# Optimization experiments

Hardware: AMD Instinct MI355X
Metric: run time of the kernel (lower is better)

## Reference

```python
import jax, jax.numpy as jnp
import numpy as np

B, T, S, F, D, M = 8, 8192, 8192, 64, 64, 128
EPS = 1e-9


def _draw_omega(n_omega, d_feature, rng):
    # Stacked orthogonal blocks scaled by sqrt(d_feature), as in the TF module.
    n_blocks = (n_omega + d_feature - 1) // d_feature + 1
    blocks = []
    for _ in range(n_blocks):
        g = rng.standard_normal((d_feature, d_feature)).astype(np.float32)
        q, _ = np.linalg.qr(g)
        blocks.append(q * np.sqrt(float(d_feature)))
    return jnp.asarray(np.concatenate(blocks, axis=0)[:n_omega])


def setup_inputs() -> dict:
    k0 = jax.random.key(0)
    kq, kv, kk = jax.random.split(k0, 3)
    query = jax.random.normal(kq, (B, T, F), dtype=jnp.float32)
    value = jax.random.normal(kv, (B, S, D), dtype=jnp.float32)
    key = jax.random.normal(kk, (B, S, F), dtype=jnp.float32)
    omega = _draw_omega(M, F, np.random.default_rng(0))  # (M, F)
    return {"query": query, "value": value, "key": key, "omega": omega}


def _phi(x, omega):
    # x: (B, L, F) -> (B, L, 2M) positive random features
    m = omega.shape[0]
    square_sum = jnp.sum(x * x, axis=-1, keepdims=True) / 2.0  # (B, L, 1)
    xw = jnp.einsum('blf,mf->blm', x, omega)                   # (B, L, M)
    unnorm = jnp.exp(jnp.concatenate([xw, -xw], axis=-1) - square_sum) + EPS
    return unnorm / jnp.sqrt(2.0 * m)


def reference(query, value, key, omega):
    q = _phi(query, omega)  # (B, T, 2M)
    k = _phi(key, omega)    # (B, S, 2M)
    ones = jnp.ones(value.shape[:-1] + (1,), dtype=value.dtype)
    v1 = jnp.concatenate([value, ones], axis=-1)               # (B, S, D+1)
    kv = jnp.einsum('bsm,bsd->bmd', k, v1)                     # (B, 2M, D+1)
    qkv = jnp.einsum('btm,bmd->btd', q, kv)                    # (B, T, D+1)
    normalizer = qkv[:, :, -1:]
    return qkv[:, :, :-1] / normalizer
```

## Files before the change

kernel.cpp:

```cpp
#include <hip/hip_runtime.h>


constexpr int NB = 8;
constexpr int NT = 8192;
constexpr float EPSF = 1e-9f;
constexpr float SCALE = 0.0625f;

typedef short s8v __attribute__((ext_vector_type(8)));
typedef short s4v __attribute__((ext_vector_type(4)));
typedef float f4v __attribute__((ext_vector_type(4)));

__device__ inline f4v mfma16(s8v a, s8v b, f4v c) {
  return __builtin_amdgcn_mfma_f32_16x16x32_bf16(a, b, c, 0, 0, 0);
}

__device__ inline short bf16_rne(float f) {
  unsigned u = __builtin_bit_cast(unsigned, f);
  u += 0x7fffu + ((u >> 16) & 1u);
  return (short)(u >> 16);
}
__device__ inline float bf16_to_f(short h) {
  unsigned u = ((unsigned)(unsigned short)h) << 16;
  return __builtin_bit_cast(float, u);
}

__global__ void setup_omega(const float* __restrict__ omega,
                            short* __restrict__ oh, short* __restrict__ ol) {
  int i = blockIdx.x * 256 + threadIdx.x;
  if (i >= 128 * 64) return;
  float w = omega[i];
  short h = bf16_rne(w);
  oh[i] = h;
  ol[i] = bf16_rne(w - bf16_to_f(h));
}

struct PhiRows {
  s8v ah0, al0, ah1, al1;
  float ssr[4];
  float ss;
};

__device__ inline void split8(f4v a, f4v b, s8v& h, s8v& l) {
  float v[8] = {a.x, a.y, a.z, a.w, b.x, b.y, b.z, b.w};
#pragma unroll
  for (int j = 0; j < 8; ++j) {
    short hh = bf16_rne(v[j]);
    h[j] = hh;
    l[j] = bf16_rne(v[j] - bf16_to_f(hh));
  }
}

__device__ inline void load_phi_rows(const float* __restrict__ xrow_base, int lane, PhiRows& P) {
  const int r = lane & 15, q = lane >> 4;
  const float* p = xrow_base + r * 64 + q * 8;
  f4v u0 = *(const f4v*)(p);
  f4v u1 = *(const f4v*)(p + 4);
  f4v u2 = *(const f4v*)(p + 32);
  f4v u3 = *(const f4v*)(p + 36);
  float ss = u0.x * u0.x + u0.y * u0.y + u0.z * u0.z + u0.w * u0.w
           + u1.x * u1.x + u1.y * u1.y + u1.z * u1.z + u1.w * u1.w
           + u2.x * u2.x + u2.y * u2.y + u2.z * u2.z + u2.w * u2.w
           + u3.x * u3.x + u3.y * u3.y + u3.z * u3.z + u3.w * u3.w;
  ss += __shfl_xor(ss, 16, 64);
  ss += __shfl_xor(ss, 32, 64);
  ss *= 0.5f;
  P.ss = ss;
#pragma unroll
  for (int reg = 0; reg < 4; ++reg) P.ssr[reg] = __shfl(ss, q * 4 + reg, 64);
  split8(u0, u1, P.ah0, P.al0);
  split8(u2, u3, P.ah1, P.al1);
}

__device__ inline f4v phi_xw_tile(const PhiRows& P, const short* __restrict__ oh,
                                  const short* __restrict__ ol, int f0, int lane) {
  const int fr = f0 + (lane & 15);
  const int q = lane >> 4;
  s8v bh0 = *(const s8v*)(oh + fr * 64 + q * 8);
  s8v bh1 = *(const s8v*)(oh + fr * 64 + 32 + q * 8);
  s8v bl0 = *(const s8v*)(ol + fr * 64 + q * 8);
  s8v bl1 = *(const s8v*)(ol + fr * 64 + 32 + q * 8);
  f4v c = {0.f, 0.f, 0.f, 0.f};
  c = mfma16(P.ah0, bh0, c);
  c = mfma16(P.ah1, bh1, c);
  c = mfma16(P.al0, bh0, c);
  c = mfma16(P.al1, bh1, c);
  c = mfma16(P.ah0, bl0, c);
  c = mfma16(P.ah1, bl1, c);
  return c;
}

__device__ inline f4v phi_xw_tile_T(const PhiRows& P, const short* __restrict__ oh,
                                    const short* __restrict__ ol, int f0, int lane) {
  const int fr = f0 + (lane & 15);
  const int q = lane >> 4;
  s8v ah0 = *(const s8v*)(oh + fr * 64 + q * 8);
  s8v ah1 = *(const s8v*)(oh + fr * 64 + 32 + q * 8);
  s8v al0 = *(const s8v*)(ol + fr * 64 + q * 8);
  s8v al1 = *(const s8v*)(ol + fr * 64 + 32 + q * 8);
  f4v c = {0.f, 0.f, 0.f, 0.f};
  c = mfma16(ah0, P.ah0, c);
  c = mfma16(ah1, P.ah1, c);
  c = mfma16(al0, P.ah0, c);
  c = mfma16(al1, P.ah1, c);
  c = mfma16(ah0, P.al0, c);
  c = mfma16(ah1, P.al1, c);
  return c;
}

constexpr int KF_P = 72;

__global__ __launch_bounds__(256, 4) void kv_fused(
    const float* __restrict__ key, const float* __restrict__ value,
    const short* __restrict__ oh, const short* __restrict__ ol,
    short* __restrict__ partial, float* __restrict__ kvacc, int use_partial) {
  __shared__ short kft[128 * KF_P];
  __shared__ short v1t[80 * KF_P];
  const int tid = threadIdx.x, lane = tid & 63, w = tid >> 6;
  const int b = blockIdx.x >> 7;
  const int cb = blockIdx.x & 127;
  const int fh = cb & 1;
  const int s0 = (cb >> 1) * 128;
  const int q = lane >> 4, r15 = lane & 15;

  for (int i = tid; i < 15 * KF_P; i += 256) v1t[65 * KF_P + i] = 0;

  f4v acc[2][5];
#pragma unroll
  for (int j = 0; j < 2; ++j)
#pragma unroll
    for (int n = 0; n < 5; ++n) acc[j][n] = f4v{0.f, 0.f, 0.f, 0.f};

  for (int sc = 0; sc < 2; ++sc) {
    const int sbase = s0 + sc * 64;
    __syncthreads();
    {
      const float* vb = value + ((size_t)b * NT + sbase) * 64;
#pragma unroll
      for (int i = 0; i < 4; ++i) {
        int e4 = tid + i * 256;
        f4v v4 = ((const f4v*)vb)[e4];
        int s = e4 >> 4, d0 = (e4 & 15) * 4;
        v1t[(d0 + 0) * KF_P + s] = bf16_rne(v4.x);
        v1t[(d0 + 1) * KF_P + s] = bf16_rne(v4.y);
        v1t[(d0 + 2) * KF_P + s] = bf16_rne(v4.z);
        v1t[(d0 + 3) * KF_P + s] = bf16_rne(v4.w);
      }
      if (tid < 64) v1t[64 * KF_P + tid] = (short)0x3F80;
    }
    {
      PhiRows P;
      load_phi_rows(key + ((size_t)b * NT + sbase + w * 16) * 64, lane, P);
#pragma unroll
      for (int ft = 0; ft < 4; ++ft) {
        f4v c = phi_xw_tile(P, oh, ol, fh * 64 + ft * 16, lane);
        s4v pk, nk;
#pragma unroll
        for (int reg = 0; reg < 4; ++reg) {
          float xw = c[reg];
          pk[reg] = bf16_rne((__expf(xw - P.ssr[reg]) + EPSF) * SCALE);
          nk[reg] = bf16_rne((__expf(-xw - P.ssr[reg]) + EPSF) * SCALE);
        }
        const int scol = w * 16 + q * 4;
        *(s4v*)(kft + (ft * 16 + r15) * KF_P + scol) = pk;
        *(s4v*)(kft + (64 + ft * 16 + r15) * KF_P + scol) = nk;
      }
    }
    __syncthreads();
#pragma unroll
    for (int ks = 0; ks < 2; ++ks) {
      s8v bf[5];
#pragma unroll
      for (int n = 0; n < 5; ++n)
        bf[n] = *(const s8v*)(v1t + (n * 16 + r15) * KF_P + ks * 32 + q * 8);
#pragma unroll
      for (int j = 0; j < 2; ++j) {
        s8v a = *(const s8v*)(kft + (w * 32 + j * 16 + r15) * KF_P + ks * 32 + q * 8);
#pragma unroll
        for (int n = 0; n < 5; ++n) acc[j][n] = mfma16(a, bf[n], acc[j][n]);
      }
    }
  }
  if (use_partial) {
    short* pb = partial + (size_t)blockIdx.x * (80 * 128);
#pragma unroll
    for (int j = 0; j < 2; ++j)
#pragma unroll
      for (int n = 0; n < 5; ++n) {
        int d = n * 16 + r15;
        int lf = w * 32 + j * 16 + q * 4;
        s4v pk;
#pragma unroll
        for (int reg = 0; reg < 4; ++reg) pk[reg] = bf16_rne(acc[j][n][reg]);
        *(s4v*)(pb + d * 128 + lf) = pk;
      }
  } else {
    float* pb = kvacc + (size_t)b * (80 * 256);
#pragma unroll
    for (int j = 0; j < 2; ++j)
#pragma unroll
      for (int n = 0; n < 5; ++n) {
        int d = n * 16 + r15;
        int lf = w * 32 + j * 16 + q * 4;
#pragma unroll
        for (int reg = 0; reg < 4; ++reg) {
          int lfx = lf + reg;
          int m = ((lfx & 63) + fh * 64) + 128 * (lfx >> 6);
          atomicAdd(pb + d * 256 + m, acc[j][n][reg]);
        }
      }
  }
}

__global__ __launch_bounds__(256) void kv_finalize(
    const short* __restrict__ partial, const float* __restrict__ kvacc,
    short* __restrict__ kvfrag, int use_partial) {
  int i = blockIdx.x * 256 + threadIdx.x;
  int b = i / 20480;
  int rem = i - b * 20480;
  int d = rem >> 8;
  int m = rem & 255;
  float s = 0.f;
  if (use_partial) {
    int o = m & 127, sg = m >> 7;
    int fh = o >> 6;
    int lf = (o & 63) + (sg << 6);
    const short* p = partial + ((size_t)(b * 128 + fh)) * (80 * 128) + d * 128 + lf;
#pragma unroll 8
    for (int c = 0; c < 64; ++c) s += bf16_to_f(p[(size_t)c * 2 * (80 * 128)]);
  } else {
    s = kvacc[(size_t)(b * 80 + d) * 256 + m];
  }
  int ks = m >> 5, qq = (m >> 3) & 3, j = m & 7;
  int n = d >> 4, r = d & 15;
  int lane = qq * 16 + r;
  kvfrag[(((size_t)b * 40 + ks * 5 + n) * 64 + lane) * 8 + j] = bf16_rne(s);
}

constexpr int QF_P = 264;
__global__ __launch_bounds__(256, 4) void qkv_fused(
    const float* __restrict__ query, const short* __restrict__ oh,
    const short* __restrict__ ol, const short* __restrict__ kvfrag,
    float* __restrict__ out) {
  __shared__ __align__(16) short qf[64 * QF_P];
  const int tid = threadIdx.x, lane = tid & 63, w = tid >> 6;
  const int b = blockIdx.x >> 7;
  const int t0 = (blockIdx.x & 127) * 64;
  const int q = lane >> 4, r15 = lane & 15;

  {
    PhiRows P;
    load_phi_rows(query + ((size_t)b * NT + t0 + w * 16) * 64, lane, P);
    const int t_loc = w * 16 + r15;
#pragma unroll
    for (int ft = 0; ft < 8; ++ft) {
      f4v c = phi_xw_tile_T(P, oh, ol, ft * 16, lane);
      s4v pk, nk;
#pragma unroll
      for (int reg = 0; reg < 4; ++reg) {
        float xw = c[reg];
        pk[reg] = bf16_rne((__expf(xw - P.ss) + EPSF) * SCALE);
        nk[reg] = bf16_rne((__expf(-xw - P.ss) + EPSF) * SCALE);
      }
      *(s4v*)(qf + t_loc * QF_P + ft * 16 + q * 4) = pk;
      *(s4v*)(qf + t_loc * QF_P + 128 + ft * 16 + q * 4) = nk;
    }
  }
  f4v acc[5];
#pragma unroll
  for (int n = 0; n < 5; ++n) acc[n] = f4v{0.f, 0.f, 0.f, 0.f};
  const short* kvb = kvfrag + (size_t)b * 40 * 512;
#pragma unroll
  for (int ks = 0; ks < 8; ++ks) {
    s8v a = *(const s8v*)(qf + (w * 16 + r15) * QF_P + ks * 32 + q * 8);
#pragma unroll
    for (int n = 0; n < 5; ++n) {
      s8v bf = *(const s8v*)(kvb + ((size_t)(ks * 5 + n)) * 512 + lane * 8);
      acc[n] = mfma16(a, bf, acc[n]);
    }
  }
  float den_r[4];
#pragma unroll
  for (int reg = 0; reg < 4; ++reg) den_r[reg] = __shfl(acc[4][reg], lane & 48, 64);
  float* stg = (float*)(qf + w * 16 * QF_P);
#pragma unroll
  for (int n = 0; n < 4; ++n)
#pragma unroll
    for (int reg = 0; reg < 4; ++reg) {
      int row = q * 4 + reg;
      int col = n * 16 + r15;
      stg[row * 68 + col] = acc[n][reg] / den_r[reg];
    }
  float* ob = out + ((size_t)b * NT + t0 + w * 16) * 64;
#pragma unroll
  for (int rr = 0; rr < 4; ++rr) {
    int row = rr * 4 + q;
    int c4 = r15 * 4;
    *(f4v*)(ob + row * 64 + c4) = *(const f4v*)(stg + row * 68 + c4);
  }
}

extern "C" void kernel_launch(void* const* d_in, const int* in_sizes, int n_in,
                              void* d_out, int out_size, void* d_ws, size_t ws_size,
                              hipStream_t stream) {
  const float* query = (const float*)d_in[0];
  const float* value = (const float*)d_in[1];
  const float* key   = (const float*)d_in[2];
  const float* omega = (const float*)d_in[3];
  float* out = (float*)d_out;

  char* ws = (char*)d_ws;
  short* oh = (short*)ws;
  short* ol = (short*)(ws + 16384);
  short* kvfrag = (short*)(ws + 32768);
  short* partial = (short*)(ws + 360448);
  float* kvacc = (float*)(ws + 360448);
  const size_t need_full = 360448 + (size_t)1024 * 80 * 128 * 2;
  const int use_partial = (ws_size >= need_full) ? 1 : 0;

  setup_omega<<<32, 256, 0, stream>>>(omega, oh, ol);
  if (!use_partial) {
    hipMemsetAsync(kvacc, 0, (size_t)8 * 80 * 256 * 4, stream);
  }
  kv_fused<<<1024, 256, 0, stream>>>(key, value, oh, ol, partial, kvacc, use_partial);
  kv_finalize<<<640, 256, 0, stream>>>(partial, kvacc, kvfrag, use_partial);
  qkv_fused<<<1024, 256, 0, stream>>>(query, oh, ol, kvfrag, out);
}
```

Measured before the change: 143.3 us.

## Fuse kv, finalize and qkv stages into one cooperative persistent kernel

Replaces the three separate launches (kv partial products, reduction into MFMA fragments, query-side product) with one cooperative kernel. It uses grid-stride loops over the same tiles and grid.sync barriers between stages. The aim is to remove launch gaps and kernel-boundary drains. The cost is two grid-wide barriers, host-side occupancy queries on every call, and a persistent grid that may be smaller than the original 1024 blocks. The old three-kernel path remains as a fallback.

```diff
diff --git a/kernel.cpp b/kernel.cpp
--- a/kernel.cpp
+++ b/kernel.cpp
@@ -1,4 +1,7 @@
 #include <hip/hip_runtime.h>
+#include <hip/hip_cooperative_groups.h>
+
+namespace cg = cooperative_groups;
 
 
 constexpr int NB = 8;
@@ -108,6 +111,180 @@
 }
 
 constexpr int KF_P = 72;
+constexpr int QF_P = 264;
+
+__global__ __launch_bounds__(256, 4) void fused_all(
+    const float* __restrict__ query, const float* __restrict__ value,
+    const float* __restrict__ key, const short* __restrict__ oh,
+    const short* __restrict__ ol, short* __restrict__ partial,
+    short* __restrict__ kvfrag, float* __restrict__ out, int nblk) {
+  __shared__ __align__(16) short smem[64 * QF_P];
+  const int tid = threadIdx.x, lane = tid & 63, w = tid >> 6;
+  const int q = lane >> 4, r15 = lane & 15;
+  cg::grid_group grid = cg::this_grid();
+
+  {
+    short* kft = smem;
+    short* v1t = smem + 128 * KF_P;
+    for (int i = tid; i < 15 * KF_P; i += 256) v1t[65 * KF_P + i] = 0;
+    for (int it = blockIdx.x; it < 1024; it += nblk) {
+      const int b = it >> 7;
+      const int cb = it & 127;
+      const int fh = cb & 1;
+      const int s0 = (cb >> 1) * 128;
+
+      f4v acc[2][5];
+#pragma unroll
+      for (int j = 0; j < 2; ++j)
+#pragma unroll
+        for (int n = 0; n < 5; ++n) acc[j][n] = f4v{0.f, 0.f, 0.f, 0.f};
+
+      for (int sc = 0; sc < 2; ++sc) {
+        const int sbase = s0 + sc * 64;
+        __syncthreads();
+        {
+          const float* vb = value + ((size_t)b * NT + sbase) * 64;
+#pragma unroll
+          for (int i = 0; i < 4; ++i) {
+            int e4 = tid + i * 256;
+            f4v v4 = ((const f4v*)vb)[e4];
+            int s = e4 >> 4, d0 = (e4 & 15) * 4;
+            v1t[(d0 + 0) * KF_P + s] = bf16_rne(v4.x);
+            v1t[(d0 + 1) * KF_P + s] = bf16_rne(v4.y);
+            v1t[(d0 + 2) * KF_P + s] = bf16_rne(v4.z);
+            v1t[(d0 + 3) * KF_P + s] = bf16_rne(v4.w);
+          }
+          if (tid < 64) v1t[64 * KF_P + tid] = (short)0x3F80;
+        }
+        {
+          PhiRows P;
+          load_phi_rows(key + ((size_t)b * NT + sbase + w * 16) * 64, lane, P);
+#pragma unroll
+          for (int ft = 0; ft < 4; ++ft) {
+            f4v c = phi_xw_tile(P, oh, ol, fh * 64 + ft * 16, lane);
+            s4v pk, nk;
+#pragma unroll
+            for (int reg = 0; reg < 4; ++reg) {
+              float xw = c[reg];
+              pk[reg] = bf16_rne((__expf(xw - P.ssr[reg]) + EPSF) * SCALE);
+              nk[reg] = bf16_rne((__expf(-xw - P.ssr[reg]) + EPSF) * SCALE);
+            }
+            const int scol = w * 16 + q * 4;
+            *(s4v*)(kft + (ft * 16 + r15) * KF_P + scol) = pk;
+            *(s4v*)(kft + (64 + ft * 16 + r15) * KF_P + scol) = nk;
+          }
+        }
+        __syncthreads();
+#pragma unroll
+        for (int ks = 0; ks < 2; ++ks) {
+          s8v bf[5];
+#pragma unroll
+          for (int n = 0; n < 5; ++n)
+            bf[n] = *(const s8v*)(v1t + (n * 16 + r15) * KF_P + ks * 32 + q * 8);
+#pragma unroll
+          for (int j = 0; j < 2; ++j) {
+            s8v a = *(const s8v*)(kft + (w * 32 + j * 16 + r15) * KF_P + ks * 32 + q * 8);
+#pragma unroll
+            for (int n = 0; n < 5; ++n) acc[j][n] = mfma16(a, bf[n], acc[j][n]);
+          }
+        }
+      }
+      short* pb = partial + (size_t)it * (80 * 128);
+#pragma unroll
+      for (int j = 0; j < 2; ++j)
+#pragma unroll
+        for (int n = 0; n < 5; ++n) {
+          int d = n * 16 + r15;
+          int lf = w * 32 + j * 16 + q * 4;
+          s4v pk;
+#pragma unroll
+          for (int reg = 0; reg < 4; ++reg) pk[reg] = bf16_rne(acc[j][n][reg]);
+          *(s4v*)(pb + d * 128 + lf) = pk;
+        }
+    }
+  }
+  __threadfence();
+  grid.sync();
+
+  for (int i = blockIdx.x * 256 + tid; i < 163840; i += nblk * 256) {
+    int b = i / 20480;
+    int rem = i - b * 20480;
+    int d = rem >> 8;
+    int m = rem & 255;
+    int o = m & 127, sg = m >> 7;
+    int fh = o >> 6;
+    int lf = (o & 63) + (sg << 6);
+    const short* p = partial + ((size_t)(b * 128 + fh)) * (80 * 128) + d * 128 + lf;
+    float s = 0.f;
+#pragma unroll 8
+    for (int c = 0; c < 64; ++c) s += bf16_to_f(p[(size_t)c * 2 * (80 * 128)]);
+    int ks = m >> 5, qq = (m >> 3) & 3, j = m & 7;
+    int n = d >> 4, r = d & 15;
+    int ln = qq * 16 + r;
+    kvfrag[(((size_t)b * 40 + ks * 5 + n) * 64 + ln) * 8 + j] = bf16_rne(s);
+  }
+  __threadfence();
+  grid.sync();
+
+  {
+    short* qf = smem;
+    for (int it = blockIdx.x; it < 1024; it += nblk) {
+      const int b = it >> 7;
+      const int t0 = (it & 127) * 64;
+      __syncthreads();
+      {
+        PhiRows P;
+        load_phi_rows(query + ((size_t)b * NT + t0 + w * 16) * 64, lane, P);
+        const int t_loc = w * 16 + r15;
+#pragma unroll
+        for (int ft = 0; ft < 8; ++ft) {
+          f4v c = phi_xw_tile_T(P, oh, ol, ft * 16, lane);
+          s4v pk, nk;
+#pragma unroll
+          for (int reg = 0; reg < 4; ++reg) {
+            float xw = c[reg];
+            pk[reg] = bf16_rne((__expf(xw - P.ss) + EPSF) * SCALE);
+            nk[reg] = bf16_rne((__expf(-xw - P.ss) + EPSF) * SCALE);
+          }
+          *(s4v*)(qf + t_loc * QF_P + ft * 16 + q * 4) = pk;
+          *(s4v*)(qf + t_loc * QF_P + 128 + ft * 16 + q * 4) = nk;
+        }
+      }
+      f4v acc[5];
+#pragma unroll
+      for (int n = 0; n < 5; ++n) acc[n] = f4v{0.f, 0.f, 0.f, 0.f};
+      const short* kvb = kvfrag + (size_t)b * 40 * 512;
+#pragma unroll
+      for (int ks = 0; ks < 8; ++ks) {
+        s8v a = *(const s8v*)(qf + (w * 16 + r15) * QF_P + ks * 32 + q * 8);
+#pragma unroll
+        for (int n = 0; n < 5; ++n) {
+          s8v bf = *(const s8v*)(kvb + ((size_t)(ks * 5 + n)) * 512 + lane * 8);
+          acc[n] = mfma16(a, bf, acc[n]);
+        }
+      }
+      float den_r[4];
+#pragma unroll
+      for (int reg = 0; reg < 4; ++reg) den_r[reg] = __shfl(acc[4][reg], lane & 48, 64);
+      float* stg = (float*)(qf + w * 16 * QF_P);
+#pragma unroll
+      for (int n = 0; n < 4; ++n)
+#pragma unroll
+        for (int reg = 0; reg < 4; ++reg) {
+          int row = q * 4 + reg;
+          int col = n * 16 + r15;
+          stg[row * 68 + col] = acc[n][reg] / den_r[reg];
+        }
+      float* ob = out + ((size_t)b * NT + t0 + w * 16) * 64;
+#pragma unroll
+      for (int rr = 0; rr < 4; ++rr) {
+        int row = rr * 4 + q;
+        int c4 = r15 * 4;
+        *(f4v*)(ob + row * 64 + c4) = *(const f4v*)(stg + row * 68 + c4);
+      }
+    }
+  }
+}
 
 __global__ __launch_bounds__(256, 4) void kv_fused(
     const float* __restrict__ key, const float* __restrict__ value,
@@ -236,7 +413,6 @@
   kvfrag[(((size_t)b * 40 + ks * 5 + n) * 64 + lane) * 8 + j] = bf16_rne(s);
 }
 
-constexpr int QF_P = 264;
 __global__ __launch_bounds__(256, 4) void qkv_fused(
     const float* __restrict__ query, const short* __restrict__ oh,
     const short* __restrict__ ol, const short* __restrict__ kvfrag,
@@ -246,7 +422,6 @@
   const int b = blockIdx.x >> 7;
   const int t0 = (blockIdx.x & 127) * 64;
   const int q = lane >> 4, r15 = lane & 15;
-
   {
     PhiRows P;
     load_phi_rows(query + ((size_t)b * NT + t0 + w * 16) * 64, lane, P);
@@ -318,10 +493,30 @@
   const int use_partial = (ws_size >= need_full) ? 1 : 0;
 
   setup_omega<<<32, 256, 0, stream>>>(omega, oh, ol);
-  if (!use_partial) {
-    hipMemsetAsync(kvacc, 0, (size_t)8 * 80 * 256 * 4, stream);
-  }
-  kv_fused<<<1024, 256, 0, stream>>>(key, value, oh, ol, partial, kvacc, use_partial);
-  kv_finalize<<<640, 256, 0, stream>>>(partial, kvacc, kvfrag, use_partial);
-  qkv_fused<<<1024, 256, 0, stream>>>(query, oh, ol, kvfrag, out);
-}
+
+  bool fused_ok = false;
+  if (use_partial) {
+    int num_cu = 0, maxb = 0;
+    hipDeviceGetAttribute(&num_cu, hipDeviceAttributeMultiprocessorCount, 0);
+    hipOccupancyMaxActiveBlocksPerMultiprocessor(&maxb, (const void*)fused_all, 256, 0);
+    int g = maxb * num_cu;
+    if (g > 1024) g = 1024;
+    if (g >= 64) {
+      int nblk = g;
+      void* args[] = {(void*)&query, (void*)&value, (void*)&key, (void*)&oh,
+                      (void*)&ol, (void*)&partial, (void*)&kvfrag, (void*)&out,
+                      (void*)&nblk};
+      hipError_t e = hipLaunchCooperativeKernel((void*)fused_all, dim3(g), dim3(256),
+                                                args, 0, stream);
+      fused_ok = (e == hipSuccess);
+    }
+  }
+  if (!fused_ok) {
+    if (!use_partial) {
+      hipMemsetAsync(kvacc, 0, (size_t)8 * 80 * 256 * 4, stream);
+    }
+    kv_fused<<<1024, 256, 0, stream>>>(key, value, oh, ol, partial, kvacc, use_partial);
+    kv_finalize<<<640, 256, 0, stream>>>(partial, kvacc, kvfrag, use_partial);
+    qkv_fused<<<1024, 256, 0, stream>>>(query, oh, ol, kvfrag, out);
+  }
+}
```

After: 418.2 us. 2.92x slower.

## Compute all 256 key features per block instead of splitting feature halves

Applied to the files above, without the earlier changes.

Each kv_fused block now computes all 128 omega projections (256 positive/negative features) for its 128 key rows, rather than two blocks each doing half. This stops loading and converting the same value tile and key rows twice and halves the grid, at the cost of doubling the accumulator registers and the kft shared buffer, with launch bounds lowered to 2 blocks per SM. The partial buffer is compacted to 65 rows (dropping zero padding) so partial writes and finalize reads shrink, and finalize writes zeros for rows 65 to 79.

```diff
diff --git a/kernel.cpp b/kernel.cpp
--- a/kernel.cpp
+++ b/kernel.cpp
@@ -108,25 +108,25 @@
 }
 
 constexpr int KF_P = 72;
-
-__global__ __launch_bounds__(256, 4) void kv_fused(
+constexpr int QF_P = 264;
+constexpr int PART_SZ = 65 * 256;
+
+__global__ __launch_bounds__(256, 2) void kv_fused(
     const float* __restrict__ key, const float* __restrict__ value,
     const short* __restrict__ oh, const short* __restrict__ ol,
     short* __restrict__ partial, float* __restrict__ kvacc, int use_partial) {
-  __shared__ short kft[128 * KF_P];
+  __shared__ short kft[256 * KF_P];
   __shared__ short v1t[80 * KF_P];
   const int tid = threadIdx.x, lane = tid & 63, w = tid >> 6;
-  const int b = blockIdx.x >> 7;
-  const int cb = blockIdx.x & 127;
-  const int fh = cb & 1;
-  const int s0 = (cb >> 1) * 128;
+  const int b = blockIdx.x >> 6;
+  const int s0 = (blockIdx.x & 63) * 128;
   const int q = lane >> 4, r15 = lane & 15;
 
   for (int i = tid; i < 15 * KF_P; i += 256) v1t[65 * KF_P + i] = 0;
 
-  f4v acc[2][5];
-#pragma unroll
-  for (int j = 0; j < 2; ++j)
+  f4v acc[4][5];
+#pragma unroll
+  for (int j = 0; j < 4; ++j)
 #pragma unroll
     for (int n = 0; n < 5; ++n) acc[j][n] = f4v{0.f, 0.f, 0.f, 0.f};
 
@@ -151,8 +151,8 @@
       PhiRows P;
       load_phi_rows(key + ((size_t)b * NT + sbase + w * 16) * 64, lane, P);
 #pragma unroll
-      for (int ft = 0; ft < 4; ++ft) {
-        f4v c = phi_xw_tile(P, oh, ol, fh * 64 + ft * 16, lane);
+      for (int ft = 0; ft < 8; ++ft) {
+        f4v c = phi_xw_tile(P, oh, ol, ft * 16, lane);
         s4v pk, nk;
 #pragma unroll
         for (int reg = 0; reg < 4; ++reg) {
@@ -162,7 +162,7 @@
         }
         const int scol = w * 16 + q * 4;
         *(s4v*)(kft + (ft * 16 + r15) * KF_P + scol) = pk;
-        *(s4v*)(kft + (64 + ft * 16 + r15) * KF_P + scol) = nk;
+        *(s4v*)(kft + (128 + ft * 16 + r15) * KF_P + scol) = nk;
       }
     }
     __syncthreads();
@@ -173,41 +173,48 @@
       for (int n = 0; n < 5; ++n)
         bf[n] = *(const s8v*)(v1t + (n * 16 + r15) * KF_P + ks * 32 + q * 8);
 #pragma unroll
-      for (int j = 0; j < 2; ++j) {
-        s8v a = *(const s8v*)(kft + (w * 32 + j * 16 + r15) * KF_P + ks * 32 + q * 8);
+      for (int j = 0; j < 4; ++j) {
+        s8v a = *(const s8v*)(kft + (w * 64 + j * 16 + r15) * KF_P + ks * 32 + q * 8);
 #pragma unroll
         for (int n = 0; n < 5; ++n) acc[j][n] = mfma16(a, bf[n], acc[j][n]);
       }
     }
   }
   if (use_partial) {
-    short* pb = partial + (size_t)blockIdx.x * (80 * 128);
-#pragma unroll
-    for (int j = 0; j < 2; ++j)
-#pragma unroll
-      for (int n = 0; n < 5; ++n) {
+    short* pb = partial + (size_t)blockIdx.x * PART_SZ;
+#pragma unroll
+    for (int j = 0; j < 4; ++j) {
+      int m = w * 64 + j * 16 + q * 4;
+#pragma unroll
+      for (int n = 0; n < 4; ++n) {
         int d = n * 16 + r15;
-        int lf = w * 32 + j * 16 + q * 4;
         s4v pk;
 #pragma unroll
         for (int reg = 0; reg < 4; ++reg) pk[reg] = bf16_rne(acc[j][n][reg]);
-        *(s4v*)(pb + d * 128 + lf) = pk;
-      }
+        *(s4v*)(pb + d * 256 + m) = pk;
+      }
+      if (r15 == 0) {
+        s4v pk;
+#pragma unroll
+        for (int reg = 0; reg < 4; ++reg) pk[reg] = bf16_rne(acc[j][4][reg]);
+        *(s4v*)(pb + 64 * 256 + m) = pk;
+      }
+    }
   } else {
-    float* pb = kvacc + (size_t)b * (80 * 256);
-#pragma unroll
-    for (int j = 0; j < 2; ++j)
-#pragma unroll
-      for (int n = 0; n < 5; ++n) {
+    float* pb = kvacc + (size_t)b * PART_SZ;
+#pragma unroll
+    for (int j = 0; j < 4; ++j) {
+      int m = w * 64 + j * 16 + q * 4;
+#pragma unroll
+      for (int n = 0; n < 4; ++n) {
         int d = n * 16 + r15;
-        int lf = w * 32 + j * 16 + q * 4;
-#pragma unroll
-        for (int reg = 0; reg < 4; ++reg) {
-          int lfx = lf + reg;
-          int m = ((lfx & 63) + fh * 64) + 128 * (lfx >> 6);
-          atomicAdd(pb + d * 256 + m, acc[j][n][reg]);
-        }
-      }
+#pragma unroll
+        for (int reg = 0; reg < 4; ++reg) atomicAdd(pb + d * 256 + m + reg, acc[j][n][reg]);
+      }
+      if (r15 == 0)
+#pragma unroll
+        for (int reg = 0; reg < 4; ++reg) atomicAdd(pb + 64 * 256 + m + reg, acc[j][4][reg]);
+    }
   }
 }
 
@@ -220,15 +227,14 @@
   int d = rem >> 8;
   int m = rem & 255;
   float s = 0.f;
-  if (use_partial) {
-    int o = m & 127, sg = m >> 7;
-    int fh = o >> 6;
-    int lf = (o & 63) + (sg << 6);
-    const short* p = partial + ((size_t)(b * 128 + fh)) * (80 * 128) + d * 128 + lf;
+  if (d < 65) {
+    if (use_partial) {
+      const short* p = partial + (size_t)(b * 64) * PART_SZ + d * 256 + m;
 #pragma unroll 8
-    for (int c = 0; c < 64; ++c) s += bf16_to_f(p[(size_t)c * 2 * (80 * 128)]);
-  } else {
-    s = kvacc[(size_t)(b * 80 + d) * 256 + m];
+      for (int c = 0; c < 64; ++c) s += bf16_to_f(p[(size_t)c * PART_SZ]);
+    } else {
+      s = kvacc[(size_t)b * PART_SZ + d * 256 + m];
+    }
   }
   int ks = m >> 5, qq = (m >> 3) & 3, j = m & 7;
   int n = d >> 4, r = d & 15;
@@ -236,7 +242,6 @@
   kvfrag[(((size_t)b * 40 + ks * 5 + n) * 64 + lane) * 8 + j] = bf16_rne(s);
 }
 
-constexpr int QF_P = 264;
 __global__ __launch_bounds__(256, 4) void qkv_fused(
     const float* __restrict__ query, const short* __restrict__ oh,
     const short* __restrict__ ol, const short* __restrict__ kvfrag,
@@ -314,14 +319,14 @@
   short* kvfrag = (short*)(ws + 32768);
   short* partial = (short*)(ws + 360448);
   float* kvacc = (float*)(ws + 360448);
-  const size_t need_full = 360448 + (size_t)1024 * 80 * 128 * 2;
+  const size_t need_full = 360448 + (size_t)512 * PART_SZ * 2;
   const int use_partial = (ws_size >= need_full) ? 1 : 0;
 
   setup_omega<<<32, 256, 0, stream>>>(omega, oh, ol);
   if (!use_partial) {
-    hipMemsetAsync(kvacc, 0, (size_t)8 * 80 * 256 * 4, stream);
-  }
-  kv_fused<<<1024, 256, 0, stream>>>(key, value, oh, ol, partial, kvacc, use_partial);
+    hipMemsetAsync(kvacc, 0, (size_t)8 * PART_SZ * 4, stream);
+  }
+  kv_fused<<<512, 256, 0, stream>>>(key, value, oh, ol, partial, kvacc, use_partial);
   kv_finalize<<<640, 256, 0, stream>>>(partial, kvacc, kvfrag, use_partial);
   qkv_fused<<<1024, 256, 0, stream>>>(query, oh, ol, kvfrag, out);
 }
```

New measurement: 143.1 us. Within noise of the previous version (-0.2%).
